# Optimization experiments

Measured on AMD Instinct MI355X. Metric: run time of the kernel, lower is better.

The kernel has to match this reference:

```python
import jax, jax.numpy as jnp
import numpy as np

D_MODEL = 1024
NUM_HEADS = 16
D_K = D_MODEL // NUM_HEADS
BATCH = 4
SEQ = 1024
NEG_INF = jnp.float32(-1e30)


def setup_inputs() -> dict:
    key = jax.random.key(0)
    ks = jax.random.split(key, 12)
    s = 1.0 / np.sqrt(D_MODEL)
    inp = {
        "Q": jax.random.normal(ks[0], (BATCH, SEQ, D_MODEL), jnp.float32),
        "K": jax.random.normal(ks[1], (BATCH, SEQ, D_MODEL), jnp.float32),
        "V": jax.random.normal(ks[2], (BATCH, SEQ, D_MODEL), jnp.float32),
        # causal mask, broadcastable [1,1,Sq,Sk]; entries==0 are masked out
        "mask": jnp.tril(jnp.ones((SEQ, SEQ), jnp.int32))[None, None],
        "W_q": jax.random.normal(ks[3], (D_MODEL, D_MODEL), jnp.float32) * s,
        "b_q": jnp.zeros((D_MODEL,), jnp.float32),
        "W_k": jax.random.normal(ks[4], (D_MODEL, D_MODEL), jnp.float32) * s,
        "b_k": jnp.zeros((D_MODEL,), jnp.float32),
        "W_v": jax.random.normal(ks[5], (D_MODEL, D_MODEL), jnp.float32) * s,
        "b_v": jnp.zeros((D_MODEL,), jnp.float32),
        "W_o": jax.random.normal(ks[6], (D_MODEL, D_MODEL), jnp.float32) * s,
        "b_o": jnp.zeros((D_MODEL,), jnp.float32),
    }
    return inp


def _split_heads(x):
    b, s, _ = x.shape
    return x.reshape(b, s, NUM_HEADS, D_K).transpose(0, 2, 1, 3)  # [b,h,s,dk]


def reference(Q, K, V, mask, W_q, b_q, W_k, b_k, W_v, b_v, W_o, b_o):
    # linear projections (torch Linear: x @ W.T + b)
    q = _split_heads(Q @ W_q.T + b_q)
    k = _split_heads(K @ W_k.T + b_k)
    v = _split_heads(V @ W_v.T + b_v)
    scale = 1.0 / jnp.sqrt(jnp.float32(D_K))
    scores = jnp.einsum("bhqd,bhkd->bhqk", q, k) * scale
    scores = jnp.where(mask == 0, NEG_INF, scores)
    attn = jax.nn.softmax(scores, axis=-1)  # dropout is identity in eval mode
    out = jnp.einsum("bhqk,bhkd->bhqd", attn, v)
    out = out.transpose(0, 2, 1, 3).reshape(Q.shape[0], Q.shape[1], D_MODEL)
    out = out @ W_o.T + b_o
    return out, attn
```

## Files before the change

### kernel.cpp

```cpp
#include <hip/hip_runtime.h>
#include <math.h>

#define SEQ 1024
#define DM  1024

typedef unsigned short u16;
typedef __attribute__((ext_vector_type(8))) short bf16x8;
typedef __attribute__((ext_vector_type(8))) unsigned short u16x8;
typedef __attribute__((ext_vector_type(4))) float f32x4;

__device__ __forceinline__ u16 f2bf(float f) {
  union { float f; unsigned int u; } x; x.f = f;
  return (u16)((x.u + 0x7fffu + ((x.u >> 16) & 1u)) >> 16);
}

__device__ __forceinline__ void gload16(const void* g, void* l) {
  __builtin_amdgcn_global_load_lds(
      (const __attribute__((address_space(1))) unsigned int*)g,
      (__attribute__((address_space(3))) unsigned int*)l, 16, 0, 0);
}

struct ConvArgs { const float* s[7]; u16* d[7]; };

__global__ __launch_bounds__(256) void conv_bf16(ConvArgs a) {
  const long long t  = (long long)blockIdx.x * 256 + threadIdx.x;
  const long long e0 = t * 8;
  const int u   = (int)(e0 >> 20);
  const int seg = (u < 12) ? (u >> 2) : (u - 9);
  const long long base = (u < 12) ? ((long long)(u >> 2) << 22) : ((long long)u << 20);
  const long long off  = e0 - base;
  const float* sp = a.s[seg] + off;
  float4 x = *(const float4*)sp;
  float4 y = *(const float4*)(sp + 4);
  u16x8 o;
  o[0]=f2bf(x.x); o[1]=f2bf(x.y); o[2]=f2bf(x.z); o[3]=f2bf(x.w);
  o[4]=f2bf(y.x); o[5]=f2bf(y.y); o[6]=f2bf(y.z); o[7]=f2bf(y.w);
  *(u16x8*)(a.d[seg] + off) = o;
}

struct GemmJob  { const u16* X; const u16* W; const float* bias; void* out; int mode; float scale; };
struct GemmJobs { GemmJob j[3]; };

__global__ __launch_bounds__(256) void gemm_bt(GemmJobs jobs, float* attn) {
  __shared__ u16 As[8192];
  __shared__ u16 Bs[8192];
  const int bid = blockIdx.x;
  const int tid = threadIdx.x;

  if (bid >= 768) {
    const int u  = bid - 768;
    const int bh = 6 + u / 15, b = u - (bh - 6) * 15;
    const int L4 = (15 - b) * 16;
    float* base = attn + (size_t)bh * SEQ * SEQ + (size_t)(b * 64) * SEQ + (b + 1) * 64;
    const f32x4 z = {0.f, 0.f, 0.f, 0.f};
    for (int r = 0; r < 64; ++r) {
      f32x4* rowp = (f32x4*)(base + (size_t)r * SEQ);
      for (int s = tid; s < L4; s += 256) rowp[s] = z;
    }
    return;
  }

  const GemmJob job = jobs.j[bid >> 8];
  const int rem = bid & 255;
  const int wave = tid >> 6, lane = tid & 63;
  const int lm = lane & 15, qd = lane >> 4;
  const int wm = wave & 1,  wn = wave >> 1;
  const int tm = (rem & 31) * 128, tn = (rem >> 5) * 128;

  f32x4 acc[4][4];
  #pragma unroll
  for (int i = 0; i < 4; i++)
    #pragma unroll
    for (int jx = 0; jx < 4; jx++) { f32x4 z = {0.f,0.f,0.f,0.f}; acc[i][jx] = z; }

  for (int kt = 0; kt < 1024; kt += 64) {
    #pragma unroll
    for (int i = 0; i < 4; i++) {
      const int s = (wave * 4 + i) * 64 + lane;
      const int r = s >> 3;
      const int c = (s & 7) ^ (r & 7);
      gload16(job.X + (size_t)(tm + r) * 1024 + kt + c * 8, As + (wave * 4 + i) * 512);
      gload16(job.W + (size_t)(tn + r) * 1024 + kt + c * 8, Bs + (wave * 4 + i) * 512);
    }
    __syncthreads();
    #pragma unroll
    for (int ks = 0; ks < 2; ks++) {
      bf16x8 af[4], bf[4];
      #pragma unroll
      for (int i = 0; i < 4; i++) {
        const int ra = wm * 64 + i * 16 + lm;
        af[i] = *(const bf16x8*)&As[ra * 64 + ((((ks << 2) | qd)) ^ (ra & 7)) * 8];
        const int rb = wn * 64 + i * 16 + lm;
        bf[i] = *(const bf16x8*)&Bs[rb * 64 + ((((ks << 2) | qd)) ^ (rb & 7)) * 8];
      }
      #pragma unroll
      for (int mi = 0; mi < 4; mi++)
        #pragma unroll
        for (int ni = 0; ni < 4; ni++)
          acc[mi][ni] = __builtin_amdgcn_mfma_f32_16x16x32_bf16(af[mi], bf[ni], acc[mi][ni], 0, 0, 0);
    }
    __syncthreads();
  }

  #pragma unroll
  for (int ni = 0; ni < 4; ni++) {
    const int n = tn + wn * 64 + ni * 16 + lm;
    const float bn = job.bias[n];
    #pragma unroll
    for (int mi = 0; mi < 4; mi++) {
      #pragma unroll
      for (int r = 0; r < 4; r++) {
        const int m = tm + wm * 64 + mi * 16 + (qd << 2) + r;
        const float v = (acc[mi][ni][r] + bn) * job.scale;
        if (job.mode == 0) {
          const int b = m >> 10, s = m & 1023, h = n >> 6, d = n & 63;
          ((u16*)job.out)[((size_t)((b << 4) + h) * 1024 + s) * 64 + d] = f2bf(v);
        } else if (job.mode == 1) {
          const int b = m >> 10, s = m & 1023, h = n >> 6, d = n & 63;
          ((u16*)job.out)[((size_t)((b << 4) + h) * 64 + d) * 1024 + s] = f2bf(v);
        } else {
          ((float*)job.out)[(size_t)m * 1024 + n] = v;
        }
      }
    }
  }
}

__global__ __launch_bounds__(256)
void attn_pass1(const u16* __restrict__ qbuf, const u16* __restrict__ kbuf,
                const u16* __restrict__ vtbuf, float* __restrict__ Linv,
                u16* __restrict__ ctx, float* __restrict__ attn) {
  __shared__ u16 P[4][512];
  const int tid = threadIdx.x, wave = tid >> 6, lane = tid & 63;
  const int bh = blockIdx.y;

  if (blockIdx.x >= 16) {
    if (bh >= 6) return;
    const int b  = blockIdx.x - 16;
    const int L4 = (15 - b) * 16;
    float* base = attn + (size_t)bh * SEQ * SEQ + (size_t)(b * 64) * SEQ + (b + 1) * 64;
    const f32x4 z = {0.f, 0.f, 0.f, 0.f};
    for (int r = 0; r < 64; ++r) {
      f32x4* rowp = (f32x4*)(base + (size_t)r * SEQ);
      for (int s = tid; s < L4; s += 256) rowp[s] = z;
    }
    return;
  }

  const int lm = lane & 15, qd = lane >> 4;
  const int qt = blockIdx.x * 4 + wave;
  const int q0 = qt * 16;
  const u16* Q  = qbuf  + (size_t)bh * SEQ * 64;
  const u16* K  = kbuf  + (size_t)bh * SEQ * 64;
  const u16* VT = vtbuf + (size_t)bh * 64 * SEQ;

  const bf16x8 qa = *(const bf16x8*)(Q + (size_t)(q0 + lm) * 64 + qd * 8);
  const bf16x8 qb = *(const bf16x8*)(Q + (size_t)(q0 + lm) * 64 + 32 + qd * 8);

  f32x4 o[4];
  float lsum[4] = {0.f, 0.f, 0.f, 0.f};
  #pragma unroll
  for (int i = 0; i < 4; i++) { f32x4 z = {0.f,0.f,0.f,0.f}; o[i] = z; }
  u16* Pw = P[wave];

  for (int kt = 0; kt < q0 + 16; kt += 32) {
    const u16* k0p = K + (size_t)(kt + lm) * 64 + qd * 8;
    const u16* k1p = K + (size_t)(kt + 16 + lm) * 64 + qd * 8;
    const bf16x8 k0a = *(const bf16x8*)k0p;
    const bf16x8 k0b = *(const bf16x8*)(k0p + 32);
    const bf16x8 k1a = *(const bf16x8*)k1p;
    const bf16x8 k1b = *(const bf16x8*)(k1p + 32);
    f32x4 s0 = {0.f,0.f,0.f,0.f}, s1 = {0.f,0.f,0.f,0.f};
    s0 = __builtin_amdgcn_mfma_f32_16x16x32_bf16(qa, k0a, s0, 0, 0, 0);
    s0 = __builtin_amdgcn_mfma_f32_16x16x32_bf16(qb, k0b, s0, 0, 0, 0);
    s1 = __builtin_amdgcn_mfma_f32_16x16x32_bf16(qa, k1a, s1, 0, 0, 0);
    s1 = __builtin_amdgcn_mfma_f32_16x16x32_bf16(qb, k1b, s1, 0, 0, 0);
    #pragma unroll
    for (int r = 0; r < 4; r++) {
      const int row = q0 + (qd << 2) + r;
      const float e0 = (kt + lm      <= row) ? __expf(s0[r]) : 0.f;
      const float e1 = (kt + 16 + lm <= row) ? __expf(s1[r]) : 0.f;
      lsum[r] += e0 + e1;
      Pw[((qd << 2) + r) * 32 + lm]      = f2bf(e0);
      Pw[((qd << 2) + r) * 32 + 16 + lm] = f2bf(e1);
    }
    const bf16x8 pf = *(const bf16x8*)&Pw[lm * 32 + qd * 8];
    #pragma unroll
    for (int db = 0; db < 4; db++) {
      const bf16x8 vf = *(const bf16x8*)(VT + (size_t)(db * 16 + lm) * SEQ + kt + qd * 8);
      o[db] = __builtin_amdgcn_mfma_f32_16x16x32_bf16(pf, vf, o[db], 0, 0, 0);
    }
  }

  const int b = bh >> 4, h = bh & 15;
  #pragma unroll
  for (int r = 0; r < 4; r++) {
    float l = lsum[r];
    l += __shfl_xor(l, 1, 16);
    l += __shfl_xor(l, 2, 16);
    l += __shfl_xor(l, 4, 16);
    l += __shfl_xor(l, 8, 16);
    const float inv = 1.0f / l;
    const int row = q0 + (qd << 2) + r;
    if (lm == 0) Linv[(size_t)bh * SEQ + row] = inv;
    #pragma unroll
    for (int db = 0; db < 4; db++) {
      const int d = db * 16 + lm;
      ctx[(size_t)(b * SEQ + row) * DM + h * 64 + d] = f2bf(o[db][r] * inv);
    }
  }
}

__global__ __launch_bounds__(256)
void attn_pass2(const u16* __restrict__ qbuf, const u16* __restrict__ kbuf,
                const float* __restrict__ Linv, float* __restrict__ attn) {
  const int tid = threadIdx.x, wave = tid >> 6, lane = tid & 63;
  const int lm = lane & 15, qd = lane >> 4;
  const int bh = blockIdx.z;
  const int q0 = blockIdx.y * 64;
  const int k0 = blockIdx.x * 256 + wave * 64;
  float* A = attn + (size_t)bh * SEQ * SEQ;

  if (k0 > q0 + 63) {
    const f32x4 z = {0.f,0.f,0.f,0.f};
    #pragma unroll
    for (int i = 0; i < 16; i++)
      *(f32x4*)&A[(size_t)(q0 + i * 4 + qd) * SEQ + k0 + lm * 4] = z;
    return;
  }

  const u16* Q = qbuf + (size_t)bh * SEQ * 64;
  const u16* K = kbuf + (size_t)bh * SEQ * 64;
  bf16x8 qf[4][2]; float invl[4];
  #pragma unroll
  for (int qs = 0; qs < 4; qs++) {
    const int qq = q0 + qs * 16;
    qf[qs][0] = *(const bf16x8*)(Q + (size_t)(qq + lm) * 64 + qd * 8);
    qf[qs][1] = *(const bf16x8*)(Q + (size_t)(qq + lm) * 64 + 32 + qd * 8);
    invl[qs]  = Linv[(size_t)bh * SEQ + qq + lm];
  }
  for (int ks = 0; ks < 4; ks++) {
    const int kk = k0 + ks * 16;
    const u16* kp = K + (size_t)(kk + lm) * 64 + qd * 8;
    const bf16x8 kf0 = *(const bf16x8*)kp;
    const bf16x8 kf1 = *(const bf16x8*)(kp + 32);
    #pragma unroll
    for (int qs = 0; qs < 4; qs++) {
      const int qq = q0 + qs * 16;
      const int kbase = kk + (qd << 2);
      f32x4 v = {0.f,0.f,0.f,0.f};
      if (kk <= qq + 15) {
        f32x4 c = {0.f,0.f,0.f,0.f};
        c = __builtin_amdgcn_mfma_f32_16x16x32_bf16(kf0, qf[qs][0], c, 0, 0, 0);
        c = __builtin_amdgcn_mfma_f32_16x16x32_bf16(kf1, qf[qs][1], c, 0, 0, 0);
        const int qg = qq + lm;
        #pragma unroll
        for (int r = 0; r < 4; r++)
          v[r] = (kbase + r <= qg) ? __expf(c[r]) * invl[qs] : 0.f;
      }
      *(f32x4*)&A[(size_t)(qq + lm) * SEQ + kbase] = v;
    }
  }
}

__global__ __launch_bounds__(256)
void gemmo_pass2(const u16* __restrict__ ctx, const u16* __restrict__ Wob,
                 const float* __restrict__ bo, float* __restrict__ out,
                 const u16* __restrict__ qbuf, const u16* __restrict__ kbuf,
                 const float* __restrict__ Linv, float* __restrict__ attn) {
  __shared__ u16 As[8192];
  __shared__ u16 Bs[8192];
  const int bid = blockIdx.x;
  const int tid = threadIdx.x, wave = tid >> 6, lane = tid & 63;
  const int lm = lane & 15, qd = lane >> 4;

  if (bid < 256) {
    const int wm = wave & 1, wn = wave >> 1;
    const int tm = (bid & 31) * 128, tn = (bid >> 5) * 128;

    f32x4 acc[4][4];
    #pragma unroll
    for (int i = 0; i < 4; i++)
      #pragma unroll
      for (int jx = 0; jx < 4; jx++) { f32x4 z = {0.f,0.f,0.f,0.f}; acc[i][jx] = z; }

    for (int kt = 0; kt < 1024; kt += 64) {
      #pragma unroll
      for (int i = 0; i < 4; i++) {
        const int s = (wave * 4 + i) * 64 + lane;
        const int r = s >> 3;
        const int c = (s & 7) ^ (r & 7);
        gload16(ctx + (size_t)(tm + r) * 1024 + kt + c * 8, As + (wave * 4 + i) * 512);
        gload16(Wob + (size_t)(tn + r) * 1024 + kt + c * 8, Bs + (wave * 4 + i) * 512);
      }
      __syncthreads();
      #pragma unroll
      for (int ks = 0; ks < 2; ks++) {
        bf16x8 af[4], bf[4];
        #pragma unroll
        for (int i = 0; i < 4; i++) {
          const int ra = wm * 64 + i * 16 + lm;
          af[i] = *(const bf16x8*)&As[ra * 64 + ((((ks << 2) | qd)) ^ (ra & 7)) * 8];
          const int rb = wn * 64 + i * 16 + lm;
          bf[i] = *(const bf16x8*)&Bs[rb * 64 + ((((ks << 2) | qd)) ^ (rb & 7)) * 8];
        }
        #pragma unroll
        for (int mi = 0; mi < 4; mi++)
          #pragma unroll
          for (int ni = 0; ni < 4; ni++)
            acc[mi][ni] = __builtin_amdgcn_mfma_f32_16x16x32_bf16(af[mi], bf[ni], acc[mi][ni], 0, 0, 0);
      }
      __syncthreads();
    }

    #pragma unroll
    for (int ni = 0; ni < 4; ni++) {
      const int n = tn + wn * 64 + ni * 16 + lm;
      const float bn = bo[n];
      #pragma unroll
      for (int mi = 0; mi < 4; mi++) {
        #pragma unroll
        for (int r = 0; r < 4; r++) {
          const int m = tm + wm * 64 + mi * 16 + (qd << 2) + r;
          out[(size_t)m * 1024 + n] = acc[mi][ni][r] + bn;
        }
      }
    }
    return;
  }

  const int p  = bid - 256;
  const int bh = p >> 6;
  const int q0 = ((p >> 2) & 15) * 64;
  const int k0 = (p & 3) * 256 + wave * 64;
  float* A = attn + (size_t)bh * SEQ * SEQ;

  if (k0 > q0 + 63) return;

  const u16* Q = qbuf + (size_t)bh * SEQ * 64;
  const u16* K = kbuf + (size_t)bh * SEQ * 64;
  bf16x8 qf[4][2]; float invl[4];
  #pragma unroll
  for (int qs = 0; qs < 4; qs++) {
    const int qq = q0 + qs * 16;
    qf[qs][0] = *(const bf16x8*)(Q + (size_t)(qq + lm) * 64 + qd * 8);
    qf[qs][1] = *(const bf16x8*)(Q + (size_t)(qq + lm) * 64 + 32 + qd * 8);
    invl[qs]  = Linv[(size_t)bh * SEQ + qq + lm];
  }
  for (int ks = 0; ks < 4; ks++) {
    const int kk = k0 + ks * 16;
    const u16* kp = K + (size_t)(kk + lm) * 64 + qd * 8;
    const bf16x8 kf0 = *(const bf16x8*)kp;
    const bf16x8 kf1 = *(const bf16x8*)(kp + 32);
    #pragma unroll
    for (int qs = 0; qs < 4; qs++) {
      const int qq = q0 + qs * 16;
      const int kbase = kk + (qd << 2);
      f32x4 v = {0.f,0.f,0.f,0.f};
      if (kk <= qq + 15) {
        f32x4 c = {0.f,0.f,0.f,0.f};
        c = __builtin_amdgcn_mfma_f32_16x16x32_bf16(kf0, qf[qs][0], c, 0, 0, 0);
        c = __builtin_amdgcn_mfma_f32_16x16x32_bf16(kf1, qf[qs][1], c, 0, 0, 0);
        const int qg = qq + lm;
        #pragma unroll
        for (int r = 0; r < 4; r++)
          v[r] = (kbase + r <= qg) ? __expf(c[r]) * invl[qs] : 0.f;
      }
      *(f32x4*)&A[(size_t)(qq + lm) * SEQ + kbase] = v;
    }
  }
}

extern "C" void kernel_launch(void* const* d_in, const int* in_sizes, int n_in,
                              void* d_out, int out_size, void* d_ws, size_t ws_size,
                              hipStream_t stream)
{
  (void)in_sizes; (void)n_in; (void)out_size;
  const float* Qf = (const float*)d_in[0];
  const float* Kf = (const float*)d_in[1];
  const float* Vf = (const float*)d_in[2];
  const float* Wq = (const float*)d_in[4];
  const float* bq = (const float*)d_in[5];
  const float* Wk = (const float*)d_in[6];
  const float* bk = (const float*)d_in[7];
  const float* Wv = (const float*)d_in[8];
  const float* bv = (const float*)d_in[9];
  const float* Wo = (const float*)d_in[10];
  const float* bo = (const float*)d_in[11];

  float* out  = (float*)d_out;
  float* attn = out + (size_t)4 * SEQ * DM;

  char* sc = (char*)attn;
  char* ob = (char*)out;
  char* ws = (char*)d_ws;

  u16* Xq = (u16*)(sc);
  u16* Xk = (u16*)(sc + (8  << 20));
  u16* Xv = (u16*)(sc + (16 << 20));

  u16* qbuf  = (u16*)ws;
  u16* kbuf  = (u16*)(ws + (8  << 20));
  u16* vtbuf = (u16*)(ws + (16 << 20));
  float* Linv = (float*)(ws + (24 << 20));

  const int big_ws = ws_size >= ((size_t)35 << 20);
  u16* ctx = big_ws ? (u16*)(ws + (25 << 20)) : (u16*)(sc + (32 << 20));
  u16* Wob = big_ws ? (u16*)(ws + (33 << 20)) : (u16*)(sc + (30 << 20));
  u16* Wqb = big_ws ? (u16*)(ob)              : (u16*)(sc + (24 << 20));
  u16* Wkb = big_ws ? (u16*)(ob + (2 << 20))  : (u16*)(sc + (26 << 20));
  u16* Wvb = big_ws ? (u16*)(ob + (4 << 20))  : (u16*)(sc + (28 << 20));

  ConvArgs ca;
  ca.s[0]=Qf; ca.s[1]=Kf; ca.s[2]=Vf; ca.s[3]=Wq; ca.s[4]=Wk; ca.s[5]=Wv; ca.s[6]=Wo;
  ca.d[0]=Xq; ca.d[1]=Xk; ca.d[2]=Xv; ca.d[3]=Wqb; ca.d[4]=Wkb; ca.d[5]=Wvb; ca.d[6]=Wob;
  conv_bf16<<<8192, 256, 0, stream>>>(ca);

  GemmJobs gj;
  gj.j[0] = (GemmJob){Xq, Wqb, bq, (void*)qbuf,  0, 0.125f};
  gj.j[1] = (GemmJob){Xk, Wkb, bk, (void*)kbuf,  0, 1.0f};
  gj.j[2] = (GemmJob){Xv, Wvb, bv, (void*)vtbuf, 1, 1.0f};
  gemm_bt<<<big_ws ? 1638 : 768, 256, 0, stream>>>(gj, attn);

  attn_pass1<<<dim3(big_ws ? 31 : 16, 64), 256, 0, stream>>>(
      qbuf, kbuf, vtbuf, Linv, ctx, attn);

  if (big_ws) {
    gemmo_pass2<<<4352, 256, 0, stream>>>(ctx, Wob, bo, out, qbuf, kbuf, Linv, attn);
  } else {
    GemmJobs go;
    go.j[0] = (GemmJob){ctx, Wob, bo, (void*)out, 2, 1.0f};
    go.j[1] = go.j[0];
    go.j[2] = go.j[0];
    gemm_bt<<<256, 256, 0, stream>>>(go, attn);
    attn_pass2<<<dim3(4, 16, 64), 256, 0, stream>>>(qbuf, kbuf, Linv, attn);
  }
}
```

Baseline: 547.8 us.

## Fuse fp32-to-bf16 activation conversion into the QKV projection GEMM

On the large-workspace path, the QKV projection GEMM now streams fp32 activations straight into shared memory and converts them to bf16 while building the MFMA fragments. This removes the separate conversion pass over Q/K/V, which wrote and then reread a bf16 copy. Only the weights are still pre-converted, by a smaller kernel. All of the upper-triangle attn zero-fill moves into the GEMM launch, which drops the zeroing blocks from attn_pass1. In exchange the A tile doubles in LDS, each k-step loads twice the bytes of activations, and the conversion arithmetic is repeated by every N-tile that reuses the same rows.

```diff
diff --git a/kernel.cpp b/kernel.cpp
--- a/kernel.cpp
+++ b/kernel.cpp
@@ -18,6 +18,22 @@
   __builtin_amdgcn_global_load_lds(
       (const __attribute__((address_space(1))) unsigned int*)g,
       (__attribute__((address_space(3))) unsigned int*)l, 16, 0, 0);
+}
+
+struct ConvWArgs { const float* s[4]; u16* d[4]; };
+
+__global__ __launch_bounds__(256) void conv_w(ConvWArgs a) {
+  const long long t  = (long long)blockIdx.x * 256 + threadIdx.x;
+  const long long e0 = t * 8;
+  const int seg = (int)(e0 >> 20);
+  const long long off = e0 - ((long long)seg << 20);
+  const float* sp = a.s[seg] + off;
+  float4 x = *(const float4*)sp;
+  float4 y = *(const float4*)(sp + 4);
+  u16x8 o;
+  o[0]=f2bf(x.x); o[1]=f2bf(x.y); o[2]=f2bf(x.z); o[3]=f2bf(x.w);
+  o[4]=f2bf(y.x); o[5]=f2bf(y.y); o[6]=f2bf(y.z); o[7]=f2bf(y.w);
+  *(u16x8*)(a.d[seg] + off) = o;
 }
 
 struct ConvArgs { const float* s[7]; u16* d[7]; };
@@ -38,18 +54,19 @@
   *(u16x8*)(a.d[seg] + off) = o;
 }
 
-struct GemmJob  { const u16* X; const u16* W; const float* bias; void* out; int mode; float scale; };
+struct GemmJob  { const u16* X; const float* Xf; const u16* W; const float* bias;
+                  void* out; int mode; float scale; };
 struct GemmJobs { GemmJob j[3]; };
 
 __global__ __launch_bounds__(256) void gemm_bt(GemmJobs jobs, float* attn) {
-  __shared__ u16 As[8192];
+  __shared__ u16 As[16384];
   __shared__ u16 Bs[8192];
   const int bid = blockIdx.x;
   const int tid = threadIdx.x;
 
   if (bid >= 768) {
     const int u  = bid - 768;
-    const int bh = 6 + u / 15, b = u - (bh - 6) * 15;
+    const int bh = u / 15, b = u - (bh * 15);
     const int L4 = (15 - b) * 16;
     float* base = attn + (size_t)bh * SEQ * SEQ + (size_t)(b * 64) * SEQ + (b + 1) * 64;
     const f32x4 z = {0.f, 0.f, 0.f, 0.f};
@@ -74,13 +91,30 @@
     for (int jx = 0; jx < 4; jx++) { f32x4 z = {0.f,0.f,0.f,0.f}; acc[i][jx] = z; }
 
   for (int kt = 0; kt < 1024; kt += 64) {
-    #pragma unroll
-    for (int i = 0; i < 4; i++) {
-      const int s = (wave * 4 + i) * 64 + lane;
-      const int r = s >> 3;
-      const int c = (s & 7) ^ (r & 7);
-      gload16(job.X + (size_t)(tm + r) * 1024 + kt + c * 8, As + (wave * 4 + i) * 512);
-      gload16(job.W + (size_t)(tn + r) * 1024 + kt + c * 8, Bs + (wave * 4 + i) * 512);
+    if (job.Xf) {
+      #pragma unroll
+      for (int i = 0; i < 8; i++) {
+        const int s = (wave * 8 + i) * 64 + lane;
+        const int r = s >> 4;
+        const int c = (s & 15) ^ (r & 7);
+        gload16(job.Xf + (size_t)(tm + r) * 1024 + kt + c * 4, As + (wave * 8 + i) * 512);
+      }
+      #pragma unroll
+      for (int i = 0; i < 4; i++) {
+        const int s = (wave * 4 + i) * 64 + lane;
+        const int r = s >> 3;
+        const int c = (s & 7) ^ (r & 7);
+        gload16(job.W + (size_t)(tn + r) * 1024 + kt + c * 8, Bs + (wave * 4 + i) * 512);
+      }
+    } else {
+      #pragma unroll
+      for (int i = 0; i < 4; i++) {
+        const int s = (wave * 4 + i) * 64 + lane;
+        const int r = s >> 3;
+        const int c = (s & 7) ^ (r & 7);
+        gload16(job.X + (size_t)(tm + r) * 1024 + kt + c * 8, As + (wave * 4 + i) * 512);
+        gload16(job.W + (size_t)(tn + r) * 1024 + kt + c * 8, Bs + (wave * 4 + i) * 512);
+      }
     }
     __syncthreads();
     #pragma unroll
@@ -89,7 +123,19 @@
       #pragma unroll
       for (int i = 0; i < 4; i++) {
         const int ra = wm * 64 + i * 16 + lm;
-        af[i] = *(const bf16x8*)&As[ra * 64 + ((((ks << 2) | qd)) ^ (ra & 7)) * 8];
+        if (job.Xf) {
+          const int c0 = (ks << 3) | (qd << 1);
+          const int s0 = ra * 16 + ((c0)     ^ (ra & 7));
+          const int s1 = ra * 16 + ((c0 + 1) ^ (ra & 7));
+          const f32x4 lo = *(const f32x4*)&As[s0 * 8];
+          const f32x4 hi = *(const f32x4*)&As[s1 * 8];
+          u16x8 o;
+          o[0]=f2bf(lo[0]); o[1]=f2bf(lo[1]); o[2]=f2bf(lo[2]); o[3]=f2bf(lo[3]);
+          o[4]=f2bf(hi[0]); o[5]=f2bf(hi[1]); o[6]=f2bf(hi[2]); o[7]=f2bf(hi[3]);
+          af[i] = *(bf16x8*)&o;
+        } else {
+          af[i] = *(const bf16x8*)&As[ra * 64 + ((((ks << 2) | qd)) ^ (ra & 7)) * 8];
+        }
         const int rb = wn * 64 + i * 16 + lm;
         bf[i] = *(const bf16x8*)&Bs[rb * 64 + ((((ks << 2) | qd)) ^ (rb & 7)) * 8];
       }
@@ -129,26 +175,12 @@
 __global__ __launch_bounds__(256)
 void attn_pass1(const u16* __restrict__ qbuf, const u16* __restrict__ kbuf,
                 const u16* __restrict__ vtbuf, float* __restrict__ Linv,
-                u16* __restrict__ ctx, float* __restrict__ attn) {
+                u16* __restrict__ ctx) {
   __shared__ u16 P[4][512];
   const int tid = threadIdx.x, wave = tid >> 6, lane = tid & 63;
-  const int bh = blockIdx.y;
-
-  if (blockIdx.x >= 16) {
-    if (bh >= 6) return;
-    const int b  = blockIdx.x - 16;
-    const int L4 = (15 - b) * 16;
-    float* base = attn + (size_t)bh * SEQ * SEQ + (size_t)(b * 64) * SEQ + (b + 1) * 64;
-    const f32x4 z = {0.f, 0.f, 0.f, 0.f};
-    for (int r = 0; r < 64; ++r) {
-      f32x4* rowp = (f32x4*)(base + (size_t)r * SEQ);
-      for (int s = tid; s < L4; s += 256) rowp[s] = z;
-    }
-    return;
-  }
-
   const int lm = lane & 15, qd = lane >> 4;
   const int qt = blockIdx.x * 4 + wave;
+  const int bh = blockIdx.y;
   const int q0 = qt * 16;
   const u16* Q  = qbuf  + (size_t)bh * SEQ * 64;
   const u16* K  = kbuf  + (size_t)bh * SEQ * 64;
@@ -395,10 +427,6 @@
   char* ob = (char*)out;
   char* ws = (char*)d_ws;
 
-  u16* Xq = (u16*)(sc);
-  u16* Xk = (u16*)(sc + (8  << 20));
-  u16* Xv = (u16*)(sc + (16 << 20));
-
   u16* qbuf  = (u16*)ws;
   u16* kbuf  = (u16*)(ws + (8  << 20));
   u16* vtbuf = (u16*)(ws + (16 << 20));
@@ -411,25 +439,40 @@
   u16* Wkb = big_ws ? (u16*)(ob + (2 << 20))  : (u16*)(sc + (26 << 20));
   u16* Wvb = big_ws ? (u16*)(ob + (4 << 20))  : (u16*)(sc + (28 << 20));
 
-  ConvArgs ca;
-  ca.s[0]=Qf; ca.s[1]=Kf; ca.s[2]=Vf; ca.s[3]=Wq; ca.s[4]=Wk; ca.s[5]=Wv; ca.s[6]=Wo;
-  ca.d[0]=Xq; ca.d[1]=Xk; ca.d[2]=Xv; ca.d[3]=Wqb; ca.d[4]=Wkb; ca.d[5]=Wvb; ca.d[6]=Wob;
-  conv_bf16<<<8192, 256, 0, stream>>>(ca);
-
-  GemmJobs gj;
-  gj.j[0] = (GemmJob){Xq, Wqb, bq, (void*)qbuf,  0, 0.125f};
-  gj.j[1] = (GemmJob){Xk, Wkb, bk, (void*)kbuf,  0, 1.0f};
-  gj.j[2] = (GemmJob){Xv, Wvb, bv, (void*)vtbuf, 1, 1.0f};
-  gemm_bt<<<big_ws ? 1638 : 768, 256, 0, stream>>>(gj, attn);
-
-  attn_pass1<<<dim3(big_ws ? 31 : 16, 64), 256, 0, stream>>>(
-      qbuf, kbuf, vtbuf, Linv, ctx, attn);
-
   if (big_ws) {
+    ConvWArgs cw;
+    cw.s[0]=Wq; cw.s[1]=Wk; cw.s[2]=Wv; cw.s[3]=Wo;
+    cw.d[0]=Wqb; cw.d[1]=Wkb; cw.d[2]=Wvb; cw.d[3]=Wob;
+    conv_w<<<2048, 256, 0, stream>>>(cw);
+
+    GemmJobs gj;
+    gj.j[0] = (GemmJob){nullptr, Qf, Wqb, bq, (void*)qbuf,  0, 0.125f};
+    gj.j[1] = (GemmJob){nullptr, Kf, Wkb, bk, (void*)kbuf,  0, 1.0f};
+    gj.j[2] = (GemmJob){nullptr, Vf, Wvb, bv, (void*)vtbuf, 1, 1.0f};
+    gemm_bt<<<1728, 256, 0, stream>>>(gj, attn);
+
+    attn_pass1<<<dim3(16, 64), 256, 0, stream>>>(qbuf, kbuf, vtbuf, Linv, ctx);
+
     gemmo_pass2<<<4352, 256, 0, stream>>>(ctx, Wob, bo, out, qbuf, kbuf, Linv, attn);
   } else {
+    u16* Xq = (u16*)(sc);
+    u16* Xk = (u16*)(sc + (8  << 20));
+    u16* Xv = (u16*)(sc + (16 << 20));
+    ConvArgs ca;
+    ca.s[0]=Qf; ca.s[1]=Kf; ca.s[2]=Vf; ca.s[3]=Wq; ca.s[4]=Wk; ca.s[5]=Wv; ca.s[6]=Wo;
+    ca.d[0]=Xq; ca.d[1]=Xk; ca.d[2]=Xv; ca.d[3]=Wqb; ca.d[4]=Wkb; ca.d[5]=Wvb; ca.d[6]=Wob;
+    conv_bf16<<<8192, 256, 0, stream>>>(ca);
+
+    GemmJobs gj;
+    gj.j[0] = (GemmJob){Xq, nullptr, Wqb, bq, (void*)qbuf,  0, 0.125f};
+    gj.j[1] = (GemmJob){Xk, nullptr, Wkb, bk, (void*)kbuf,  0, 1.0f};
+    gj.j[2] = (GemmJob){Xv, nullptr, Wvb, bv, (void*)vtbuf, 1, 1.0f};
+    gemm_bt<<<768, 256, 0, stream>>>(gj, attn);
+
+    attn_pass1<<<dim3(16, 64), 256, 0, stream>>>(qbuf, kbuf, vtbuf, Linv, ctx);
+
     GemmJobs go;
-    go.j[0] = (GemmJob){ctx, Wob, bo, (void*)out, 2, 1.0f};
+    go.j[0] = (GemmJob){ctx, nullptr, Wob, bo, (void*)out, 2, 1.0f};
     go.j[1] = go.j[0];
     go.j[2] = go.j[0];
     gemm_bt<<<256, 256, 0, stream>>>(go, attn);
```

Result: slower. 602.1 us (+9.9%).
